# Optimization experiments

Hardware: AMD Instinct MI355X
Metric: run time of the kernel (lower is better)

## Reference

```python
import jax, jax.numpy as jnp
import numpy as np

B, T, C = 512, 256, 384   # batch, seq (== block_size), n_embd
HS, BS = 64, 256          # head_size, block_size


def setup_inputs() -> dict:
    key = jax.random.key(0)
    ks = jax.random.split(key, 6)
    s = 1.0 / np.sqrt(C)
    s2 = 1.0 / np.sqrt(HS)
    return {
        "x": jax.random.normal(ks[0], (B, T, C), jnp.float32),
        "W_q": jax.random.normal(ks[1], (C, HS), jnp.float32) * s,
        "W_k": jax.random.normal(ks[2], (C, HS), jnp.float32) * s,
        "W_v": jax.random.normal(ks[3], (C, HS), jnp.float32) * s,
        "W_ql": jax.random.normal(ks[4], (HS, BS), jnp.float32) * s2,
        "W_kl": jax.random.normal(ks[5], (HS, BS), jnp.float32) * s2,
    }


def reference(x, W_q, W_k, W_v, W_ql, W_kl):
    # One head of self-attention, additive (tanh) score variant, eval mode.
    # x: [B,T,C]
    q = jnp.einsum("btc,ch->bth", x, W_q)          # [B,T,HS]
    k = jnp.einsum("btc,ch->bth", x, W_k)          # [B,T,HS]
    q_w = jnp.einsum("bth,hs->bts", q, W_ql)       # [B,T,BS]
    k_w = jnp.einsum("bth,hs->bts", k, W_kl)       # [B,T,BS]
    # NOTE: elementwise add (both [B,T,BS]) as in the torch code, then tanh.
    wei = jnp.tanh(q_w + k_w)                      # [B,T,T] since T == BS
    Tn = x.shape[1]
    causal = jnp.tril(jnp.ones((Tn, Tn), dtype=bool))
    wei = jnp.where(causal, wei, -jnp.inf)
    wei = jax.nn.softmax(wei, axis=-1)
    v = jnp.einsum("btc,ch->bth", x, W_v)          # [B,T,HS]
    out = jnp.einsum("bts,bsh->bth", wei, v)       # [B,T,HS]
    return out
```

## Files before the change

kernel.cpp:

```cpp
#include <hip/hip_runtime.h>

#define BATCH 512
#define TT    256
#define CC    384
#define HH    64
#define NCOL  320

typedef float  f32x4 __attribute__((ext_vector_type(4)));
typedef short  s16x8 __attribute__((ext_vector_type(8)));

#define X_OFF   0
#define W_OFF   16384
#define P_OFF   36864
#define V_OFF   110592
#define RS_OFF  143360
#define LDS_TOTAL 145408

__device__ __forceinline__ unsigned short f2bf(float f) {
    union { float f; unsigned u; } c; c.f = f;
    unsigned u = c.u;
    u += 0x7fffu + ((u >> 16) & 1u);
    return (unsigned short)(u >> 16);
}

__device__ __forceinline__ int prefix_of(int rt) {
    int a = rt >> 1, bb = rt & 1;
    return rt + a * (a - 1) + bb * a;
}

__global__ void prep_w(const float* __restrict__ Wq, const float* __restrict__ Wk,
                       const float* __restrict__ Wv, const float* __restrict__ Wql,
                       const float* __restrict__ Wkl, unsigned short* __restrict__ wsW) {
    int gid = blockIdx.x * 256 + threadIdx.x;
    int k, n; float val;
    if (gid < CC * 256) {
        k = gid >> 8; int s = gid & 255; n = s;
        float acc = 0.f;
        for (int h = 0; h < HH; ++h)
            acc += Wq[k * HH + h] * Wql[h * 256 + s] + Wk[k * HH + h] * Wkl[h * 256 + s];
        val = acc;
    } else {
        int g2 = gid - CC * 256;
        k = g2 >> 6; int h = g2 & 63; n = 256 + h;
        val = Wv[k * HH + h];
    }
    int kc = k >> 5, ct = n >> 4;
    int lane = ((k >> 3) & 3) * 16 + (n & 15);
    int j = k & 7;
    wsW[(((kc * 20 + ct) * 64) + lane) * 8 + j] = f2bf(val);
}

__global__ __launch_bounds__(512) void head_main(const float* __restrict__ x,
                                                 const unsigned short* __restrict__ wsW,
                                                 float* __restrict__ out) {
    extern __shared__ char sm[];
    unsigned short* Xs = (unsigned short*)(sm + X_OFF);
    unsigned short* Ws = (unsigned short*)(sm + W_OFF);
    unsigned short* Pb = (unsigned short*)(sm + P_OFF);
    unsigned short* Vb = (unsigned short*)(sm + V_OFF);
    float*          rs = (float*)(sm + RS_OFF);

    const int b    = blockIdx.x;
    const int t    = threadIdx.x;
    const int w    = t >> 6;
    const int lane = t & 63;
    const int cgrp = w >> 2;
    const int iw   = w & 3;
    const int q    = lane >> 4;
    const int cidx = lane & 15;
    const int rts[4] = { iw, 7 - iw, 8 + iw, 15 - iw };
    const int rtmax  = 15 - iw;

    f32x4 acc[4][10];
#pragma unroll
    for (int a = 0; a < 4; ++a)
#pragma unroll
        for (int c2 = 0; c2 < 10; ++c2) acc[a][c2] = (f32x4){0.f, 0.f, 0.f, 0.f};

    const float* xb = x + (size_t)b * (TT * CC);

    for (int kc = 0; kc < 12; ++kc) {
        __syncthreads();
#pragma unroll
        for (int ssi = 0; ssi < 2; ++ssi) {
            int slot = t + ssi * 512;
            int rt = slot >> 6, L = slot & 63;
            int row  = rt * 16 + (L & 15);
            int koff = (L >> 4) * 8;
            const float4* src = (const float4*)(xb + row * CC + kc * 32 + koff);
            float4 f0 = src[0], f1 = src[1];
            s16x8 v;
            v[0] = (short)f2bf(f0.x); v[1] = (short)f2bf(f0.y);
            v[2] = (short)f2bf(f0.z); v[3] = (short)f2bf(f0.w);
            v[4] = (short)f2bf(f1.x); v[5] = (short)f2bf(f1.y);
            v[6] = (short)f2bf(f1.z); v[7] = (short)f2bf(f1.w);
            *(s16x8*)(Xs + slot * 8) = v;
        }
        {
            const float4* src = (const float4*)(wsW + (size_t)kc * (20 * 64 * 8));
            float4* dst = (float4*)Ws;
            dst[t]        = src[t];
            dst[t + 512]  = src[t + 512];
            if (t < 256) dst[t + 1024] = src[t + 1024];
        }
        __syncthreads();

        s16x8 af[4];
#pragma unroll
        for (int ri = 0; ri < 4; ++ri)
            af[ri] = *(const s16x8*)(Xs + (rts[ri] * 64 + lane) * 8);
#pragma unroll
        for (int cc2 = 0; cc2 < 10; ++cc2) {
            int ctg = cgrp * 10 + cc2;
            if (ctg <= 15 && ctg > rtmax) continue;
            s16x8 bf = *(const s16x8*)(Ws + (ctg * 64 + lane) * 8);
#pragma unroll
            for (int ri = 0; ri < 4; ++ri) {
                if (ctg >= 16 || ctg <= rts[ri])
                    acc[ri][cc2] = __builtin_amdgcn_mfma_f32_16x16x32_bf16(af[ri], bf, acc[ri][cc2], 0, 0, 0);
            }
        }
    }

    float rsum[4][4];
#pragma unroll
    for (int ri = 0; ri < 4; ++ri)
#pragma unroll
        for (int rg = 0; rg < 4; ++rg) rsum[ri][rg] = 0.f;

#pragma unroll
    for (int ri = 0; ri < 4; ++ri) {
        int rt = rts[ri];
#pragma unroll
        for (int cc2 = 0; cc2 < 10; ++cc2) {
            int ctg = cgrp * 10 + cc2;
            if (ctg >= 16) continue;
            if ((ctg >> 1) > (rt >> 1)) continue;
            int tix = prefix_of(rt) + (ctg >> 1);
#pragma unroll
            for (int rg = 0; rg < 4; ++rg) {
                int row = rt * 16 + q * 4 + rg;
                int col = ctg * 16 + cidx;
                float e = 0.f;
                if (col <= row) {
                    float sv = acc[ri][cc2][rg];
                    float ex = __expf(2.f * sv);
                    float th = 1.f - 2.f / (ex + 1.f);
                    e = __expf(th);
                }
                rsum[ri][rg] += e;
                int sl = col & 31;
                Pb[(tix * 64 + (sl >> 3) * 16 + (row & 15)) * 8 + (sl & 7)] = f2bf(e);
            }
        }
        if (cgrp == 1) {
#pragma unroll
            for (int cc2 = 6; cc2 < 10; ++cc2) {
                int vct = cc2 - 6;
#pragma unroll
                for (int rg = 0; rg < 4; ++rg) {
                    int srow = rt * 16 + q * 4 + rg;
                    int kcv = srow >> 5;
                    Vb[((vct * 8 + kcv) * 64 + ((srow >> 3) & 3) * 16 + cidx) * 8 + (srow & 7)] =
                        f2bf(acc[ri][cc2][rg]);
                }
            }
        }
#pragma unroll
        for (int rg = 0; rg < 4; ++rg) {
            float v = rsum[ri][rg];
            v += __shfl_xor(v, 1);
            v += __shfl_xor(v, 2);
            v += __shfl_xor(v, 4);
            v += __shfl_xor(v, 8);
            if (cidx == 0) rs[cgrp * 256 + rt * 16 + q * 4 + rg] = v;
        }
    }
    __syncthreads();

    const int r2s[2] = { w, 15 - w };
    f32x4 acc2[2][4];
#pragma unroll
    for (int r2 = 0; r2 < 2; ++r2)
#pragma unroll
        for (int ct = 0; ct < 4; ++ct) acc2[r2][ct] = (f32x4){0.f, 0.f, 0.f, 0.f};

    const int kcmax = (15 - w) >> 1;
    for (int kc = 0; kc <= kcmax; ++kc) {
        s16x8 vb[4];
#pragma unroll
        for (int ct = 0; ct < 4; ++ct)
            vb[ct] = *(const s16x8*)(Vb + ((ct * 8 + kc) * 64 + lane) * 8);
#pragma unroll
        for (int r2 = 0; r2 < 2; ++r2) {
            int rt = r2s[r2];
            if (kc <= (rt >> 1)) {
                s16x8 pf = *(const s16x8*)(Pb + ((prefix_of(rt) + kc) * 64 + lane) * 8);
#pragma unroll
                for (int ct = 0; ct < 4; ++ct)
                    acc2[r2][ct] = __builtin_amdgcn_mfma_f32_16x16x32_bf16(pf, vb[ct], acc2[r2][ct], 0, 0, 0);
            }
        }
    }

    float* ob = out + (size_t)b * (TT * HH);
#pragma unroll
    for (int r2 = 0; r2 < 2; ++r2) {
        int rt = r2s[r2];
#pragma unroll
        for (int rg = 0; rg < 4; ++rg) {
            int row = rt * 16 + q * 4 + rg;
            float inv = 1.f / (rs[row] + rs[256 + row]);
#pragma unroll
            for (int ct = 0; ct < 4; ++ct)
                ob[row * HH + ct * 16 + cidx] = acc2[r2][ct][rg] * inv;
        }
    }
}

extern "C" void kernel_launch(void* const* d_in, const int* in_sizes, int n_in,
                              void* d_out, int out_size, void* d_ws, size_t ws_size,
                              hipStream_t stream) {
    const float* x   = (const float*)d_in[0];
    const float* Wq  = (const float*)d_in[1];
    const float* Wk  = (const float*)d_in[2];
    const float* Wv  = (const float*)d_in[3];
    const float* Wql = (const float*)d_in[4];
    const float* Wkl = (const float*)d_in[5];
    unsigned short* wsW = (unsigned short*)d_ws;
    float* out = (float*)d_out;

    prep_w<<<480, 256, 0, stream>>>(Wq, Wk, Wv, Wql, Wkl, wsW);

    hipFuncSetAttribute((const void*)head_main,
                        hipFuncAttributeMaxDynamicSharedMemorySize, LDS_TOTAL);
    head_main<<<BATCH, 512, LDS_TOTAL, stream>>>(x, wsW, out);
}
```

Baseline: 341.6 us.

## Restructure attention kernel: per-wave row pairs, double-buffered async weight loads, register P

```diff
diff --git a/kernel.cpp b/kernel.cpp
--- a/kernel.cpp
+++ b/kernel.cpp
@@ -4,17 +4,15 @@
 #define TT    256
 #define CC    384
 #define HH    64
-#define NCOL  320
 
 typedef float  f32x4 __attribute__((ext_vector_type(4)));
 typedef short  s16x8 __attribute__((ext_vector_type(8)));
 
-#define X_OFF   0
-#define W_OFF   16384
-#define P_OFF   36864
-#define V_OFF   110592
-#define RS_OFF  143360
-#define LDS_TOTAL 145408
+#define XS_OFF   0
+#define WS_OFF   32768
+#define VB_OFF   114688
+#define SCR_OFF  147456
+#define LDS_TOTAL 155648
 
 __device__ __forceinline__ unsigned short f2bf(float f) {
     union { float f; unsigned u; } c; c.f = f;
@@ -23,9 +21,11 @@
     return (unsigned short)(u >> 16);
 }
 
-__device__ __forceinline__ int prefix_of(int rt) {
-    int a = rt >> 1, bb = rt & 1;
-    return rt + a * (a - 1) + bb * a;
+__device__ __forceinline__ void gld_lds16(const void* g, void* l) {
+    __builtin_amdgcn_global_load_lds(
+        (const __attribute__((address_space(1))) unsigned int*)(unsigned long long)g,
+        (__attribute__((address_space(3))) unsigned int*)(unsigned int)(unsigned long long)l,
+        16, 0, 0);
 }
 
 __global__ void prep_w(const float* __restrict__ Wq, const float* __restrict__ Wk,
@@ -44,176 +44,234 @@
         k = g2 >> 6; int h = g2 & 63; n = 256 + h;
         val = Wv[k * HH + h];
     }
-    int kc = k >> 5, ct = n >> 4;
+    int kc = k >> 6, kk = (k >> 5) & 1, ct = n >> 4;
     int lane = ((k >> 3) & 3) * 16 + (n & 15);
     int j = k & 7;
-    wsW[(((kc * 20 + ct) * 64) + lane) * 8 + j] = f2bf(val);
-}
-
-__global__ __launch_bounds__(512) void head_main(const float* __restrict__ x,
-                                                 const unsigned short* __restrict__ wsW,
-                                                 float* __restrict__ out) {
+    wsW[((((kc * 2 + kk) * 20 + ct) * 64) + lane) * 8 + j] = f2bf(val);
+}
+
+__global__ __launch_bounds__(512, 2) void head_main(const float* __restrict__ x,
+                                                    const unsigned short* __restrict__ wsW,
+                                                    float* __restrict__ out) {
     extern __shared__ char sm[];
-    unsigned short* Xs = (unsigned short*)(sm + X_OFF);
-    unsigned short* Ws = (unsigned short*)(sm + W_OFF);
-    unsigned short* Pb = (unsigned short*)(sm + P_OFF);
-    unsigned short* Vb = (unsigned short*)(sm + V_OFF);
-    float*          rs = (float*)(sm + RS_OFF);
+    unsigned short* Xs  = (unsigned short*)(sm + XS_OFF);
+    unsigned short* Wsh = (unsigned short*)(sm + WS_OFF);
+    unsigned short* Vb  = (unsigned short*)(sm + VB_OFF);
 
     const int b    = blockIdx.x;
     const int t    = threadIdx.x;
-    const int w    = t >> 6;
+    const int w    = (t >> 6) & 7;
     const int lane = t & 63;
-    const int cgrp = w >> 2;
-    const int iw   = w & 3;
     const int q    = lane >> 4;
     const int cidx = lane & 15;
-    const int rts[4] = { iw, 7 - iw, 8 + iw, 15 - iw };
-    const int rtmax  = 15 - iw;
-
-    f32x4 acc[4][10];
-#pragma unroll
-    for (int a = 0; a < 4; ++a)
-#pragma unroll
-        for (int c2 = 0; c2 < 10; ++c2) acc[a][c2] = (f32x4){0.f, 0.f, 0.f, 0.f};
+    const int rt0  = w;
+    const int rt1  = 15 - w;
+    unsigned short* scr = (unsigned short*)(sm + SCR_OFF) + w * 512;
 
     const float* xb = x + (size_t)b * (TT * CC);
 
-    for (int kc = 0; kc < 12; ++kc) {
-        __syncthreads();
-#pragma unroll
-        for (int ssi = 0; ssi < 2; ++ssi) {
-            int slot = t + ssi * 512;
-            int rt = slot >> 6, L = slot & 63;
-            int row  = rt * 16 + (L & 15);
-            int koff = (L >> 4) * 8;
-            const float4* src = (const float4*)(xb + row * CC + kc * 32 + koff);
-            float4 f0 = src[0], f1 = src[1];
+    f32x4 accS0[8], accS1[16], accV[2][4];
+#pragma unroll
+    for (int i = 0; i < 8; ++i)  accS0[i] = (f32x4){0.f,0.f,0.f,0.f};
+#pragma unroll
+    for (int i = 0; i < 16; ++i) accS1[i] = (f32x4){0.f,0.f,0.f,0.f};
+#pragma unroll
+    for (int i = 0; i < 2; ++i)
+#pragma unroll
+        for (int j = 0; j < 4; ++j) accV[i][j] = (f32x4){0.f,0.f,0.f,0.f};
+
+    int xrow[4], xkoff[4];
+#pragma unroll
+    for (int i = 0; i < 4; ++i) {
+        int g = t + i * 512;
+        int kk = g >> 10, rt = (g >> 6) & 15, L = g & 63;
+        xrow[i]  = rt * 16 + (L & 15);
+        xkoff[i] = kk * 32 + ((L >> 4) & 3) * 8;
+    }
+
+    float4 xf[8];
+#pragma unroll
+    for (int i = 0; i < 4; ++i) {
+        const float4* p = (const float4*)(xb + xrow[i] * CC + xkoff[i]);
+        xf[2*i]   = p[0];
+        xf[2*i+1] = p[1];
+    }
+#pragma unroll
+    for (int i = 0; i < 5; ++i) {
+        int g = t + i * 512;
+        gld_lds16(wsW + g * 8, Wsh + g * 8);
+    }
+
+    for (int kc = 0; kc < 6; ++kc) {
+#pragma unroll
+        for (int i = 0; i < 4; ++i) {
+            int g = t + i * 512;
+            float4 f0 = xf[2*i], f1 = xf[2*i+1];
             s16x8 v;
             v[0] = (short)f2bf(f0.x); v[1] = (short)f2bf(f0.y);
             v[2] = (short)f2bf(f0.z); v[3] = (short)f2bf(f0.w);
             v[4] = (short)f2bf(f1.x); v[5] = (short)f2bf(f1.y);
             v[6] = (short)f2bf(f1.z); v[7] = (short)f2bf(f1.w);
-            *(s16x8*)(Xs + slot * 8) = v;
-        }
-        {
-            const float4* src = (const float4*)(wsW + (size_t)kc * (20 * 64 * 8));
-            float4* dst = (float4*)Ws;
-            dst[t]        = src[t];
-            dst[t + 512]  = src[t + 512];
-            if (t < 256) dst[t + 1024] = src[t + 1024];
+            *(s16x8*)(Xs + g * 8) = v;
         }
         __syncthreads();
 
-        s16x8 af[4];
-#pragma unroll
-        for (int ri = 0; ri < 4; ++ri)
-            af[ri] = *(const s16x8*)(Xs + (rts[ri] * 64 + lane) * 8);
-#pragma unroll
-        for (int cc2 = 0; cc2 < 10; ++cc2) {
-            int ctg = cgrp * 10 + cc2;
-            if (ctg <= 15 && ctg > rtmax) continue;
-            s16x8 bf = *(const s16x8*)(Ws + (ctg * 64 + lane) * 8);
-#pragma unroll
-            for (int ri = 0; ri < 4; ++ri) {
-                if (ctg >= 16 || ctg <= rts[ri])
-                    acc[ri][cc2] = __builtin_amdgcn_mfma_f32_16x16x32_bf16(af[ri], bf, acc[ri][cc2], 0, 0, 0);
-            }
-        }
-    }
-
-    float rsum[4][4];
-#pragma unroll
-    for (int ri = 0; ri < 4; ++ri)
-#pragma unroll
-        for (int rg = 0; rg < 4; ++rg) rsum[ri][rg] = 0.f;
-
-#pragma unroll
-    for (int ri = 0; ri < 4; ++ri) {
-        int rt = rts[ri];
-#pragma unroll
-        for (int cc2 = 0; cc2 < 10; ++cc2) {
-            int ctg = cgrp * 10 + cc2;
-            if (ctg >= 16) continue;
-            if ((ctg >> 1) > (rt >> 1)) continue;
-            int tix = prefix_of(rt) + (ctg >> 1);
+        if (kc < 5) {
+            const int kn = kc + 1;
+#pragma unroll
+            for (int i = 0; i < 4; ++i) {
+                const float4* p = (const float4*)(xb + xrow[i] * CC + kn * 64 + xkoff[i]);
+                xf[2*i]   = p[0];
+                xf[2*i+1] = p[1];
+            }
+            const unsigned short* wsrc = wsW + (size_t)kn * 20480;
+            unsigned short*       wdst = Wsh + (kn & 1) * 20480;
+#pragma unroll
+            for (int i = 0; i < 5; ++i) {
+                int g = t + i * 512;
+                gld_lds16(wsrc + g * 8, wdst + g * 8);
+            }
+        }
+
+        const unsigned short* Wb = Wsh + (kc & 1) * 20480;
+#pragma unroll
+        for (int kk = 0; kk < 2; ++kk) {
+            s16x8 a0 = *(const s16x8*)(Xs + ((kk * 16 + rt0) * 64 + lane) * 8);
+            s16x8 a1 = *(const s16x8*)(Xs + ((kk * 16 + rt1) * 64 + lane) * 8);
+#pragma unroll
+            for (int ct = 0; ct < 16; ++ct) {
+                if (ct <= rt1) {
+                    s16x8 bf = *(const s16x8*)(Wb + ((kk * 20 + ct) * 64 + lane) * 8);
+                    accS1[ct] = __builtin_amdgcn_mfma_f32_16x16x32_bf16(a1, bf, accS1[ct], 0, 0, 0);
+                    if (ct < 8 && ct <= rt0)
+                        accS0[ct] = __builtin_amdgcn_mfma_f32_16x16x32_bf16(a0, bf, accS0[ct], 0, 0, 0);
+                }
+            }
+#pragma unroll
+            for (int v2 = 0; v2 < 4; ++v2) {
+                s16x8 bf = *(const s16x8*)(Wb + ((kk * 20 + 16 + v2) * 64 + lane) * 8);
+                accV[0][v2] = __builtin_amdgcn_mfma_f32_16x16x32_bf16(a0, bf, accV[0][v2], 0, 0, 0);
+                accV[1][v2] = __builtin_amdgcn_mfma_f32_16x16x32_bf16(a1, bf, accV[1][v2], 0, 0, 0);
+            }
+        }
+        __syncthreads();
+    }
+
+    float rs0[4] = {0.f,0.f,0.f,0.f}, rs1[4] = {0.f,0.f,0.f,0.f};
+    s16x8 pf0[4], pf1[8];
+
+#pragma unroll
+    for (int ch = 0; ch < 8; ++ch) {
+        if (ch <= (rt1 >> 1)) {
+#pragma unroll
+            for (int sub = 0; sub < 2; ++sub) {
+                const int ct = 2 * ch + sub;
+                const int gcol = ct * 16 + cidx;
+                const int c = sub * 16 + cidx;
+#pragma unroll
+                for (int rg = 0; rg < 4; ++rg) {
+                    const int grow = rt1 * 16 + q * 4 + rg;
+                    float e = 0.f;
+                    if (ct <= rt1 && gcol <= grow) {
+                        float sv = accS1[2 * ch + sub][rg];
+                        float ex = __expf(2.f * sv);
+                        float th = 1.f - __fdividef(2.f, ex + 1.f);
+                        e = __expf(th);
+                    }
+                    rs1[rg] += e;
+                    scr[((c >> 3) * 16 + q * 4 + rg) * 8 + (c & 7)] = f2bf(e);
+                }
+            }
+            pf1[ch] = *(const s16x8*)(scr + lane * 8);
+        }
+    }
+#pragma unroll
+    for (int ch = 0; ch < 4; ++ch) {
+        if (ch <= (rt0 >> 1)) {
+#pragma unroll
+            for (int sub = 0; sub < 2; ++sub) {
+                const int ct = 2 * ch + sub;
+                const int gcol = ct * 16 + cidx;
+                const int c = sub * 16 + cidx;
+#pragma unroll
+                for (int rg = 0; rg < 4; ++rg) {
+                    const int grow = rt0 * 16 + q * 4 + rg;
+                    float e = 0.f;
+                    if (ct <= rt0 && gcol <= grow) {
+                        float sv = accS0[2 * ch + sub][rg];
+                        float ex = __expf(2.f * sv);
+                        float th = 1.f - __fdividef(2.f, ex + 1.f);
+                        e = __expf(th);
+                    }
+                    rs0[rg] += e;
+                    scr[((c >> 3) * 16 + q * 4 + rg) * 8 + (c & 7)] = f2bf(e);
+                }
+            }
+            pf0[ch] = *(const s16x8*)(scr + lane * 8);
+        }
+    }
+
+#pragma unroll
+    for (int ri = 0; ri < 2; ++ri) {
+        const int rt = ri ? rt1 : rt0;
+#pragma unroll
+        for (int vct = 0; vct < 4; ++vct)
 #pragma unroll
             for (int rg = 0; rg < 4; ++rg) {
-                int row = rt * 16 + q * 4 + rg;
-                int col = ctg * 16 + cidx;
-                float e = 0.f;
-                if (col <= row) {
-                    float sv = acc[ri][cc2][rg];
-                    float ex = __expf(2.f * sv);
-                    float th = 1.f - 2.f / (ex + 1.f);
-                    e = __expf(th);
-                }
-                rsum[ri][rg] += e;
-                int sl = col & 31;
-                Pb[(tix * 64 + (sl >> 3) * 16 + (row & 15)) * 8 + (sl & 7)] = f2bf(e);
-            }
-        }
-        if (cgrp == 1) {
-#pragma unroll
-            for (int cc2 = 6; cc2 < 10; ++cc2) {
-                int vct = cc2 - 6;
-#pragma unroll
-                for (int rg = 0; rg < 4; ++rg) {
-                    int srow = rt * 16 + q * 4 + rg;
-                    int kcv = srow >> 5;
-                    Vb[((vct * 8 + kcv) * 64 + ((srow >> 3) & 3) * 16 + cidx) * 8 + (srow & 7)] =
-                        f2bf(acc[ri][cc2][rg]);
-                }
-            }
-        }
-#pragma unroll
-        for (int rg = 0; rg < 4; ++rg) {
-            float v = rsum[ri][rg];
-            v += __shfl_xor(v, 1);
-            v += __shfl_xor(v, 2);
-            v += __shfl_xor(v, 4);
-            v += __shfl_xor(v, 8);
-            if (cidx == 0) rs[cgrp * 256 + rt * 16 + q * 4 + rg] = v;
-        }
-    }
+                int srow = rt * 16 + q * 4 + rg;
+                Vb[((vct * 8 + (srow >> 5)) * 64 + ((srow >> 3) & 3) * 16 + cidx) * 8 + (srow & 7)] =
+                    f2bf(accV[ri][vct][rg]);
+            }
+    }
+
+#pragma unroll
+    for (int rg = 0; rg < 4; ++rg) {
+        float v0 = rs0[rg], v1 = rs1[rg];
+        v0 += __shfl_xor(v0, 1); v0 += __shfl_xor(v0, 2);
+        v0 += __shfl_xor(v0, 4); v0 += __shfl_xor(v0, 8);
+        v1 += __shfl_xor(v1, 1); v1 += __shfl_xor(v1, 2);
+        v1 += __shfl_xor(v1, 4); v1 += __shfl_xor(v1, 8);
+        rs0[rg] = v0; rs1[rg] = v1;
+    }
+
     __syncthreads();
 
-    const int r2s[2] = { w, 15 - w };
     f32x4 acc2[2][4];
 #pragma unroll
-    for (int r2 = 0; r2 < 2; ++r2)
-#pragma unroll
-        for (int ct = 0; ct < 4; ++ct) acc2[r2][ct] = (f32x4){0.f, 0.f, 0.f, 0.f};
-
-    const int kcmax = (15 - w) >> 1;
-    for (int kc = 0; kc <= kcmax; ++kc) {
-        s16x8 vb[4];
-#pragma unroll
-        for (int ct = 0; ct < 4; ++ct)
-            vb[ct] = *(const s16x8*)(Vb + ((ct * 8 + kc) * 64 + lane) * 8);
-#pragma unroll
-        for (int r2 = 0; r2 < 2; ++r2) {
-            int rt = r2s[r2];
-            if (kc <= (rt >> 1)) {
-                s16x8 pf = *(const s16x8*)(Pb + ((prefix_of(rt) + kc) * 64 + lane) * 8);
-#pragma unroll
-                for (int ct = 0; ct < 4; ++ct)
-                    acc2[r2][ct] = __builtin_amdgcn_mfma_f32_16x16x32_bf16(pf, vb[ct], acc2[r2][ct], 0, 0, 0);
+    for (int i = 0; i < 2; ++i)
+#pragma unroll
+        for (int j = 0; j < 4; ++j) acc2[i][j] = (f32x4){0.f,0.f,0.f,0.f};
+
+    const int nch0 = rt0 >> 1, nch1 = rt1 >> 1;
+#pragma unroll
+    for (int ch = 0; ch < 8; ++ch) {
+        if (ch <= nch1) {
+            s16x8 vb[4];
+#pragma unroll
+            for (int vct = 0; vct < 4; ++vct)
+                vb[vct] = *(const s16x8*)(Vb + ((vct * 8 + ch) * 64 + lane) * 8);
+#pragma unroll
+            for (int vct = 0; vct < 4; ++vct)
+                acc2[1][vct] = __builtin_amdgcn_mfma_f32_16x16x32_bf16(pf1[ch], vb[vct], acc2[1][vct], 0, 0, 0);
+            if (ch < 4 && ch <= nch0) {
+#pragma unroll
+                for (int vct = 0; vct < 4; ++vct)
+                    acc2[0][vct] = __builtin_amdgcn_mfma_f32_16x16x32_bf16(pf0[ch], vb[vct], acc2[0][vct], 0, 0, 0);
             }
         }
     }
 
     float* ob = out + (size_t)b * (TT * HH);
 #pragma unroll
-    for (int r2 = 0; r2 < 2; ++r2) {
-        int rt = r2s[r2];
+    for (int ri = 0; ri < 2; ++ri) {
+        const int rt = ri ? rt1 : rt0;
 #pragma unroll
         for (int rg = 0; rg < 4; ++rg) {
             int row = rt * 16 + q * 4 + rg;
-            float inv = 1.f / (rs[row] + rs[256 + row]);
-#pragma unroll
-            for (int ct = 0; ct < 4; ++ct)
-                ob[row * HH + ct * 16 + cidx] = acc2[r2][ct][rg] * inv;
+            float inv = __fdividef(1.f, ri ? rs1[rg] : rs0[rg]);
+#pragma unroll
+            for (int vct = 0; vct < 4; ++vct)
+                ob[row * HH + vct * 16 + cidx] = acc2[ri][vct][rg] * inv;
         }
     }
 }
```

Result: faster. 321.0 us (-6.0%).
